# Optimization experiments

Hardware: AMD Instinct MI355X
Metric: run time of the kernel (lower is better)

The kernel has to match this reference:

```python
import jax, jax.numpy as jnp
import numpy as np
import math

B, C, H, W = 8, 512, 32, 32
NUM_GROUPS = 32
NUM_HEADS = C // 64  # num_head_channels=64 -> 8 heads
EPS = 1e-5


def setup_inputs() -> dict:
    key = jax.random.key(0)
    ks = jax.random.split(key, 7)
    x = jax.random.normal(ks[0], (B, C, H, W), dtype=jnp.float32)
    gn_w = jax.random.uniform(ks[1], (C,), dtype=jnp.float32, minval=0.5, maxval=1.5)
    gn_b = jax.random.normal(ks[2], (C,), dtype=jnp.float32) * 0.1
    qkv_w = jax.random.normal(ks[3], (3 * C, C), dtype=jnp.float32) * 0.02
    qkv_b = jax.random.normal(ks[4], (3 * C,), dtype=jnp.float32) * 0.02
    proj_w = jax.random.normal(ks[5], (C, C), dtype=jnp.float32) * 0.02
    proj_b = jax.random.normal(ks[6], (C,), dtype=jnp.float32) * 0.02
    return {"x": x, "gn_w": gn_w, "gn_b": gn_b, "qkv_w": qkv_w,
            "qkv_b": qkv_b, "proj_w": proj_w, "proj_b": proj_b}


def _group_norm(x, w, b):
    # x: [B, C, L]
    bb, cc, ll = x.shape
    g = x.reshape(bb, NUM_GROUPS, cc // NUM_GROUPS, ll)
    mean = g.mean(axis=(2, 3), keepdims=True)
    var = g.var(axis=(2, 3), keepdims=True)
    g = (g - mean) * jax.lax.rsqrt(var + EPS)
    return g.reshape(bb, cc, ll) * w[None, :, None] + b[None, :, None]


def reference(x, gn_w, gn_b, qkv_w, qkv_b, proj_w, proj_b):
    b, c, h, w = x.shape
    L = h * w
    xf = x.reshape(b, c, L)
    # 1x1 conv1d QKV on normalized input: weight [3C, C]
    qkv = jnp.einsum('oc,bcl->bol', qkv_w, _group_norm(xf, gn_w, gn_b)) + qkv_b[None, :, None]
    ch = c // NUM_HEADS  # per-head channels
    qkv = qkv.reshape(b * NUM_HEADS, 3 * ch, L)
    q, k, v = qkv[:, :ch], qkv[:, ch:2 * ch], qkv[:, 2 * ch:]
    scale = 1.0 / math.sqrt(math.sqrt(ch))
    # [b*H, T, S] scores, softmax over source dim (computed in fp32 per source)
    weight = jnp.einsum('bct,bcs->bts', q * scale, k * scale)
    weight = jax.nn.softmax(weight.astype(jnp.float32), axis=-1).astype(weight.dtype)
    a = jnp.einsum('bts,bcs->bct', weight, v).reshape(b, c, L)
    hproj = jnp.einsum('oc,bcl->bol', proj_w, a) + proj_b[None, :, None]
    return (xf + hproj).reshape(b, c, h, w)
```

## Files before the change

kernel.cpp:

```cpp
#include <hip/hip_runtime.h>
#include <math.h>

#define BB 8
#define CC 512
#define LL 1024
#define GG 32
#define CPG 16
#define NH 8
#define CH 64

typedef unsigned short ushort_t;
typedef __attribute__((ext_vector_type(8))) short short8;
typedef __attribute__((ext_vector_type(4))) float f32x4;
typedef __attribute__((ext_vector_type(16))) float f32x16;

#define SCALE_Q 0.18033688f

__device__ inline ushort_t f2bf(float f) {
  union { float f; unsigned u; } v;
  v.f = f;
  unsigned r = v.u + 0x7FFFu + ((v.u >> 16) & 1u);
  return (ushort_t)(r >> 16);
}

__device__ inline unsigned pack_bf2(float lo, float hi) {
  return __builtin_amdgcn_perm(__float_as_uint(hi), __float_as_uint(lo),
                               0x07060302u);
}

__device__ inline int swz(int r, int k) {
  return r * 64 + ((((k >> 3) ^ (r & 7)) << 3) | (k & 7));
}

__device__ inline int vswz(int c, int s) {
  return c * 128 + (s & 64) + ((((s >> 3) & 7) ^ (c & 7)) << 3) + (s & 7);
}

__device__ __forceinline__ void g2l16(const void* g, void* l) {
  __builtin_amdgcn_global_load_lds((const unsigned int*)g, (unsigned int*)l,
                                   16, 0, 0);
}

__global__ __launch_bounds__(512) void gnx_kernel(
    const float* __restrict__ x, const float* __restrict__ gn_w,
    const float* __restrict__ gn_b, const float* __restrict__ qkv_w,
    const float* __restrict__ proj_w, ushort_t* __restrict__ xnT,
    ushort_t* __restrict__ wq, ushort_t* __restrict__ wp) {
  if (blockIdx.x < BB * GG) {
    const int b = blockIdx.x / GG;
    const int g = blockIdx.x % GG;
    const int tid = threadIdx.x;
    const int ch = tid >> 5;
    const int lseg = tid & 31;
    __shared__ ushort_t Ts[1024 * 32];
    __shared__ float red[16];
    __shared__ float st[2];
    const float* xc = x + ((size_t)b * CC + (size_t)g * CPG + ch) * LL;
    float4 v[8];
    float sum = 0.f, sq = 0.f;
#pragma unroll
    for (int i = 0; i < 8; ++i) {
      v[i] = *(const float4*)(xc + lseg * 32 + i * 4);
      sum += (v[i].x + v[i].y) + (v[i].z + v[i].w);
      sq += (v[i].x * v[i].x + v[i].y * v[i].y) +
            (v[i].z * v[i].z + v[i].w * v[i].w);
    }
#pragma unroll
    for (int off = 32; off > 0; off >>= 1) {
      sum += __shfl_down(sum, off);
      sq += __shfl_down(sq, off);
    }
    const int wave = tid >> 6;
    if ((tid & 63) == 0) {
      red[wave] = sum;
      red[8 + wave] = sq;
    }
    __syncthreads();
    if (tid == 0) {
      float s = 0.f, q = 0.f;
#pragma unroll
      for (int i = 0; i < 8; ++i) {
        s += red[i];
        q += red[8 + i];
      }
      float mean = s * (1.f / (CPG * LL));
      float var = q * (1.f / (CPG * LL)) - mean * mean;
      st[0] = mean;
      st[1] = rsqrtf(var + 1e-5f);
    }
    __syncthreads();
    const int c = g * CPG + ch;
    const float sc = st[1] * gn_w[c];
    const float sh = gn_b[c] - st[0] * sc;
    const int chG = ch >> 3, ch7 = ch & 7;
#pragma unroll
    for (int i = 0; i < 8; ++i) {
      float vv[4] = {v[i].x, v[i].y, v[i].z, v[i].w};
#pragma unroll
      for (int j = 0; j < 4; ++j) {
        int l = lseg * 32 + i * 4 + j;
        int key = ((l >> 5) + (l >> 2)) & 3;
        int slot = (chG + key) & 3;
        Ts[l * 32 + slot * 8 + ch7] = f2bf(vv[j] * sc + sh);
      }
    }
    __syncthreads();
    const int cb64 = (g >> 2) * 64;
    const int grpb = (g & 3) * 2;
#pragma unroll
    for (int it = 0; it < 4; ++it) {
      int idx = tid + it * 512;
      int l = idx >> 1, gsel = idx & 1;
      int key = ((l >> 5) + (l >> 2)) & 3;
      int slot = (gsel + key) & 3;
      uint4 val = *(const uint4*)&Ts[l * 32 + slot * 8];
      int grp = (grpb + gsel) ^ (l & 7);
      *(uint4*)(xnT + ((size_t)b * LL + l) * CC + cb64 + grp * 8) = val;
    }
  } else {
    int cb = blockIdx.x - BB * GG;
    int idx = (cb * 512 + threadIdx.x) * 4;
    const int N1 = 3 * CC * CC;
    float4 v;
    ushort_t* mat;
    int row, k;
    if (idx < N1) {
      v = *(const float4*)(qkv_w + idx);
      row = idx >> 9;
      k = idx & 511;
      mat = wq + (size_t)row * CC;
    } else {
      int j = idx - N1;
      v = *(const float4*)(proj_w + j);
      row = j >> 9;
      k = j & 511;
      mat = wp + (size_t)row * CC;
    }
    int dcol = (k & ~63) | ((((k >> 3) & 7) ^ (row & 7)) << 3) | (k & 7);
    unsigned lo = f2bf(v.x) | ((unsigned)f2bf(v.y) << 16);
    unsigned hi = f2bf(v.z) | ((unsigned)f2bf(v.w) << 16);
    *(uint2*)(mat + dcol) = make_uint2(lo, hi);
  }
}

__global__ __launch_bounds__(384, 3) void qkv_mfma_kernel(
    const ushort_t* __restrict__ wq, const ushort_t* __restrict__ xnT,
    const float* __restrict__ qkv_b, ushort_t* __restrict__ qT,
    ushort_t* __restrict__ kT, ushort_t* __restrict__ vbuf) {
  const int b = blockIdx.z;
  const int m0 = blockIdx.y * 192;
  const int n0 = blockIdx.x * 128;
  const int tid = threadIdx.x;
  const int w = tid >> 6, lane = tid & 63;
  const int col = lane & 15, quad = lane >> 4;
  const int wm = (w >> 1) * 64, wn = (w & 1) * 64;
  __shared__ ushort_t Smem[2 * 20480];
  f32x4 acc[4][4];
  f32x4 z = {0.f, 0.f, 0.f, 0.f};
#pragma unroll
  for (int i = 0; i < 4; ++i)
#pragma unroll
    for (int j = 0; j < 4; ++j) acc[i][j] = z;

  const ushort_t* arow = wq + (size_t)m0 * CC;
  const ushort_t* brow = xnT + ((size_t)b * LL + n0) * CC;

  auto stage = [&](int bb, int k0) {
    ushort_t* As = Smem + bb * 20480;
    ushort_t* Bs = As + 12288;
#pragma unroll
    for (int j = 0; j < 4; ++j) {
      int e = (j * 6 + w) * 512 + lane * 8;
      g2l16(arow + (size_t)(e >> 6) * CC + k0 + (e & 63),
            As + (j * 6 + w) * 512);
    }
    if (w < 4) {
#pragma unroll
      for (int j = 0; j < 4; ++j) {
        int e = (j * 4 + w) * 512 + lane * 8;
        g2l16(brow + (size_t)(e >> 6) * CC + k0 + (e & 63),
              Bs + (j * 4 + w) * 512);
      }
    }
  };

  stage(0, 0);
  __syncthreads();
  int cur = 0;
  for (int step = 0; step < 8; ++step) {
    if (step < 7) stage(cur ^ 1, (step + 1) * 64);
    const ushort_t* As = Smem + cur * 20480;
    const ushort_t* Bs = As + 12288;
#pragma unroll
    for (int kk = 0; kk < 2; ++kk) {
      short8 af[4], bf[4];
#pragma unroll
      for (int mi = 0; mi < 4; ++mi)
        af[mi] = *(const short8*)&As[swz(wm + mi * 16 + col, kk * 32 + quad * 8)];
#pragma unroll
      for (int ni = 0; ni < 4; ++ni)
        bf[ni] = *(const short8*)&Bs[swz(wn + ni * 16 + col, kk * 32 + quad * 8)];
#pragma unroll
      for (int mi = 0; mi < 4; ++mi)
#pragma unroll
        for (int ni = 0; ni < 4; ++ni)
          acc[mi][ni] = __builtin_amdgcn_mfma_f32_16x16x32_bf16(
              af[mi], bf[ni], acc[mi][ni], 0, 0, 0);
    }
    __syncthreads();
    cur ^= 1;
  }
  const int ci_w = w >> 1;
  ushort_t* Tile = Smem + ci_w * 8192;
  if (ci_w < 2) {
    const float sc = (ci_w == 0) ? SCALE_Q : 1.f;
#pragma unroll
    for (int mi = 0; mi < 4; ++mi) {
      int mg = m0 + wm + mi * 16 + quad * 4;
      float b0 = qkv_b[mg + 0], b1 = qkv_b[mg + 1];
      float b2 = qkv_b[mg + 2], b3 = qkv_b[mg + 3];
      int ch = mi * 16 + quad * 4;
#pragma unroll
      for (int ni = 0; ni < 4; ++ni) {
        int lloc = wn + ni * 16 + col;
        float v0 = (acc[mi][ni][0] + b0) * sc;
        float v1 = (acc[mi][ni][1] + b1) * sc;
        float v2 = (acc[mi][ni][2] + b2) * sc;
        float v3 = (acc[mi][ni][3] + b3) * sc;
        int chs = ch ^ ((lloc & 7) << 3);
        *(uint2*)&Tile[lloc * 64 + chs] =
            make_uint2(pack_bf2(v0, v1), pack_bf2(v2, v3));
      }
    }
  } else {
#pragma unroll
    for (int mi = 0; mi < 4; ++mi)
#pragma unroll
      for (int r = 0; r < 4; ++r) {
        int ch = mi * 16 + quad * 4 + r;
        float bias = qkv_b[m0 + wm + ch];
#pragma unroll
        for (int ni = 0; ni < 4; ++ni) {
          int lloc = wn + ni * 16 + col;
          Tile[ch * 128 + lloc] =
              (ushort_t)(__float_as_uint(acc[mi][ni][r] + bias) >> 16);
        }
      }
  }
  __syncthreads();
  const int head = blockIdx.y;
  const int bh = b * NH + head;
#pragma unroll
  for (int ci = 0; ci < 3; ++ci) {
    ushort_t* T2 = Smem + ci * 8192;
    if (ci < 2) {
      ushort_t* dst = (ci == 0) ? qT : kT;
#pragma unroll
      for (int it = 0; it < 3; ++it) {
        int idx = tid + it * 384;
        if (idx < 1024) {
          int l = idx >> 3, seg = idx & 7;
          uint4 v = *(const uint4*)&T2[l * 64 + seg * 8];
          *(uint4*)(dst + ((size_t)bh * LL + n0 + l) * CH + seg * 8) = v;
        }
      }
    } else {
#pragma unroll
      for (int it = 0; it < 3; ++it) {
        int idx = tid + it * 384;
        if (idx < 1024) {
          int ch = idx >> 4, lseg = idx & 15;
          uint4 v = *(const uint4*)&T2[ch * 128 + lseg * 8];
          int g = lseg & 7, blk = lseg >> 3;
          *(uint4*)(vbuf + ((size_t)bh * CH + ch) * LL + n0 + blk * 64 +
                    ((g ^ (ch & 7)) << 3)) = v;
        }
      }
    }
  }
}

__global__ __launch_bounds__(256) void attn_mfma_kernel(
    const ushort_t* __restrict__ qT, const ushort_t* __restrict__ kT,
    const ushort_t* __restrict__ vbuf, ushort_t* __restrict__ abuf) {
  const int Bx = blockIdx.x;
  const int bh = (Bx & 7) * 8 + ((Bx >> 3) >> 3);
  const int t0g = ((Bx >> 3) & 7) * 128;
  const int b = bh >> 3, h = bh & 7;
  const int tid = threadIdx.x;
  const int w = tid >> 6, lane = tid & 63;
  const int ln31 = lane & 31, hi = lane >> 5;
  __shared__ ushort_t Ksm[2][128 * 64];
  __shared__ ushort_t Vsm[2][64 * 128];

  const ushort_t* kbase = kT + (size_t)bh * LL * CH;
  const ushort_t* vbase = vbuf + (size_t)bh * CH * LL;

#pragma unroll
  for (int i = 0; i < 4; ++i) {
    int e = i * 2048 + w * 512 + lane * 8;
    g2l16(kbase + e, &Ksm[0][i * 2048 + w * 512]);
    g2l16(vbase + (size_t)(e >> 7) * LL + (e & 127),
          &Vsm[0][i * 2048 + w * 512]);
  }
  const ushort_t* qtile = qT + ((size_t)bh * LL + t0g) * CH;
  short8 bq[4];
#pragma unroll
  for (int j = 0; j < 4; ++j)
    bq[j] = *(const short8*)&qtile[swz(w * 32 + ln31, j * 16 + hi * 8)];

  union { unsigned u[4]; short8 s; } onesu;
#pragma unroll
  for (int i = 0; i < 4; ++i) onesu.u[i] = 0x3F803F80u;
  const short8 bones = onesu.s;

  float m_s = 0.f;
  f32x16 oacc[2], osum;
  f32x16 zz = {0.f, 0.f, 0.f, 0.f, 0.f, 0.f, 0.f, 0.f,
               0.f, 0.f, 0.f, 0.f, 0.f, 0.f, 0.f, 0.f};
  oacc[0] = zz;
  oacc[1] = zz;
  osum = zz;
  __syncthreads();

  int cur = 0;
  for (int it2 = 0; it2 < 8; ++it2) {
    if (it2 < 7) {
#pragma unroll
      for (int i = 0; i < 4; ++i) {
        int e = i * 2048 + w * 512 + lane * 8;
        g2l16(kbase + (size_t)(it2 + 1) * 8192 + e,
              &Ksm[cur ^ 1][i * 2048 + w * 512]);
        g2l16(vbase + (size_t)(e >> 7) * LL + (it2 + 1) * 128 + (e & 127),
              &Vsm[cur ^ 1][i * 2048 + w * 512]);
      }
    }
    const ushort_t* Kc = Ksm[cur];
    const ushort_t* Vc = Vsm[cur];
#pragma unroll
    for (int h2 = 0; h2 < 2; ++h2) {
      f32x16 sacc[2];
      sacc[0] = zz;
      sacc[1] = zz;
      __builtin_amdgcn_s_setprio(1);
#pragma unroll
      for (int sq = 0; sq < 2; ++sq)
#pragma unroll
        for (int j = 0; j < 4; ++j) {
          short8 ak = *(const short8*)&Kc[swz(h2 * 64 + sq * 32 + ln31,
                                              j * 16 + hi * 8)];
          sacc[sq] = __builtin_amdgcn_mfma_f32_32x32x16_bf16(ak, bq[j],
                                                             sacc[sq], 0, 0, 0);
        }
      __builtin_amdgcn_s_setprio(0);
      if (it2 == 0 && h2 == 0) {
        float mx = sacc[0][0];
#pragma unroll
        for (int sq = 0; sq < 2; ++sq)
#pragma unroll
          for (int r = 0; r < 16; ++r) mx = fmaxf(mx, sacc[sq][r]);
#pragma unroll
        for (int off = 32; off > 0; off >>= 1)
          mx = fmaxf(mx, __shfl_xor(mx, off));
        m_s = mx;
      }
      short8 pf[4];
#pragma unroll
      for (int sq = 0; sq < 2; ++sq) {
        float p[16];
#pragma unroll
        for (int r = 0; r < 16; ++r)
          p[r] = __builtin_amdgcn_exp2f(sacc[sq][r] - m_s);
        unsigned d0[4], d1[4];
#pragma unroll
        for (int q = 0; q < 4; ++q) {
          d0[q] = pack_bf2(p[q * 4 + 0], p[q * 4 + 1]);
          d1[q] = pack_bf2(p[q * 4 + 2], p[q * 4 + 3]);
        }
#pragma unroll
        for (int m = 0; m < 2; ++m) {
          unsigned x0 = d0[m * 2], y0 = d0[m * 2 + 1];
          unsigned x1 = d1[m * 2], y1 = d1[m * 2 + 1];
          asm volatile("v_permlane32_swap_b32 %0, %1" : "+v"(x0), "+v"(y0));
          asm volatile("v_permlane32_swap_b32 %0, %1" : "+v"(x1), "+v"(y1));
          union { uint4 u; short8 s; } fu;
          fu.u = make_uint4(x0, x1, y0, y1);
          pf[sq * 2 + m] = fu.s;
        }
      }
      __builtin_amdgcn_s_setprio(1);
#pragma unroll
      for (int cq = 0; cq < 2; ++cq)
#pragma unroll
        for (int ks = 0; ks < 4; ++ks) {
          short8 bv = *(const short8*)&Vc[vswz(cq * 32 + ln31,
                                               h2 * 64 + ks * 16 + hi * 8)];
          oacc[cq] = __builtin_amdgcn_mfma_f32_32x32x16_bf16(pf[ks], bv,
                                                             oacc[cq], 0, 0, 0);
        }
#pragma unroll
      for (int ks = 0; ks < 4; ++ks)
        osum = __builtin_amdgcn_mfma_f32_32x32x16_bf16(pf[ks], bones, osum,
                                                       0, 0, 0);
      __builtin_amdgcn_s_setprio(0);
    }
    __syncthreads();
    cur ^= 1;
  }
#pragma unroll
  for (int r = 0; r < 16; ++r) {
    int tl = (r & 3) + 8 * (r >> 2) + 4 * hi;
    float li = 1.f / osum[r];
    int lg = t0g + w * 32 + tl;
#pragma unroll
    for (int cq = 0; cq < 2; ++cq) {
      int cl = cq * 32 + ln31;
      int dcol = ((((cl >> 3) ^ (lg & 7)) << 3) | (cl & 7));
      abuf[((size_t)b * LL + lg) * CC + h * CH + dcol] =
          f2bf(oacc[cq][r] * li);
    }
  }
}

__global__ __launch_bounds__(256) void proj_mfma_kernel(
    const ushort_t* __restrict__ wp, const ushort_t* __restrict__ abuf,
    const float* __restrict__ proj_b, const float* __restrict__ x,
    float* __restrict__ out) {
  const int b = blockIdx.z;
  const int m0 = blockIdx.y * 64;
  const int n0 = blockIdx.x * 128;
  const int tid = threadIdx.x;
  const int w = tid >> 6, lane = tid & 63;
  const int col = lane & 15, quad = lane >> 4;
  const int wm = (w >> 1) * 32, wn = (w & 1) * 64;
  __shared__ ushort_t Smem[2 * 12288];
  f32x4 acc[2][4];
  f32x4 z = {0.f, 0.f, 0.f, 0.f};
#pragma unroll
  for (int i = 0; i < 2; ++i)
#pragma unroll
    for (int j = 0; j < 4; ++j) acc[i][j] = z;

  const ushort_t* arow = wp + (size_t)m0 * CC;
  const ushort_t* brow = abuf + ((size_t)b * LL + n0) * CC;

  auto stage = [&](int bb, int k0) {
    ushort_t* As = Smem + bb * 12288;
    ushort_t* Bs = As + 4096;
#pragma unroll
    for (int j = 0; j < 2; ++j) {
      int e = (j * 4 + w) * 512 + lane * 8;
      g2l16(arow + (size_t)(e >> 6) * CC + k0 + (e & 63),
            As + (j * 4 + w) * 512);
    }
#pragma unroll
    for (int j = 0; j < 4; ++j) {
      int e = (j * 4 + w) * 512 + lane * 8;
      g2l16(brow + (size_t)(e >> 6) * CC + k0 + (e & 63),
            Bs + (j * 4 + w) * 512);
    }
  };

  stage(0, 0);
  __syncthreads();
  int cur = 0;
  for (int step = 0; step < 8; ++step) {
    if (step < 7) stage(cur ^ 1, (step + 1) * 64);
    const ushort_t* As = Smem + cur * 12288;
    const ushort_t* Bs = As + 4096;
#pragma unroll
    for (int kk = 0; kk < 2; ++kk) {
      short8 af[2], bf[4];
#pragma unroll
      for (int mi = 0; mi < 2; ++mi)
        af[mi] = *(const short8*)&As[swz(wm + mi * 16 + col, kk * 32 + quad * 8)];
#pragma unroll
      for (int ni = 0; ni < 4; ++ni)
        bf[ni] = *(const short8*)&Bs[swz(wn + ni * 16 + col, kk * 32 + quad * 8)];
#pragma unroll
      for (int mi = 0; mi < 2; ++mi)
#pragma unroll
        for (int ni = 0; ni < 4; ++ni)
          acc[mi][ni] = __builtin_amdgcn_mfma_f32_16x16x32_bf16(
              af[mi], bf[ni], acc[mi][ni], 0, 0, 0);
    }
    __syncthreads();
    cur ^= 1;
  }
#pragma unroll
  for (int mi = 0; mi < 2; ++mi)
#pragma unroll
    for (int r = 0; r < 4; ++r) {
      int o = m0 + wm + mi * 16 + quad * 4 + r;
      float bias = proj_b[o];
#pragma unroll
      for (int ni = 0; ni < 4; ++ni) {
        int l = n0 + wn + ni * 16 + col;
        size_t off = ((size_t)b * CC + o) * LL + l;
        out[off] = x[off] + bias + acc[mi][ni][r];
      }
    }
}

extern "C" void kernel_launch(void* const* d_in, const int* in_sizes, int n_in,
                              void* d_out, int out_size, void* d_ws,
                              size_t ws_size, hipStream_t stream) {
  const float* x = (const float*)d_in[0];
  const float* gn_w = (const float*)d_in[1];
  const float* gn_b = (const float*)d_in[2];
  const float* qkv_w = (const float*)d_in[3];
  const float* qkv_b = (const float*)d_in[4];
  const float* proj_w = (const float*)d_in[5];
  const float* proj_b = (const float*)d_in[6];
  float* out = (float*)d_out;

  char* ws = (char*)d_ws;
  ushort_t* wq = (ushort_t*)ws;
  ushort_t* wp = wq + (size_t)3 * CC * CC;
  ushort_t* xnT = wp + (size_t)CC * CC;
  ushort_t* qT = xnT + (size_t)BB * LL * CC;
  ushort_t* kT = qT + (size_t)BB * NH * LL * CH;
  ushort_t* vb = kT + (size_t)BB * NH * LL * CH;
  ushort_t* abuf = vb + (size_t)BB * NH * LL * CH;

  gnx_kernel<<<BB * GG + 512, 512, 0, stream>>>(x, gn_w, gn_b, qkv_w, proj_w,
                                                xnT, wq, wp);
  qkv_mfma_kernel<<<dim3(LL / 128, 1536 / 192, BB), 384, 0, stream>>>(
      wq, xnT, qkv_b, qT, kT, vb);
  attn_mfma_kernel<<<dim3(512), 256, 0, stream>>>(qT, kT, vb, abuf);
  proj_mfma_kernel<<<dim3(LL / 128, CC / 64, BB), 256, 0, stream>>>(
      wp, abuf, proj_b, x, out);
}
```

Baseline: 138.5 us.

## Use 4-stage K=32 LDS pipeline with 32-wide swizzle in QKV and proj GEMMs

Both GEMM kernels change from a double-buffered K=64 loop with full __syncthreads to a four-buffer ring of K=32 slices. Three slices are kept in flight, paced by explicit vmcnt waits and a single s_barrier per step. The global swizzle of xnT, the weights and abuf moves to a 32-column XOR pattern to match the new LDS tile width. The aim is to hide global-to-LDS latency better and cut barrier cost. In exchange there are twice as many loop iterations and hand-tuned vmcnt counts that must exactly match the number of outstanding loads.

```diff
diff --git a/kernel.cpp b/kernel.cpp
--- a/kernel.cpp
+++ b/kernel.cpp
@@ -16,6 +16,8 @@
 
 #define SCALE_Q 0.18033688f
 
+#define VMW(N) asm volatile("s_waitcnt vmcnt(" #N ")" ::: "memory")
+
 __device__ inline ushort_t f2bf(float f) {
   union { float f; unsigned u; } v;
   v.f = f;
@@ -30,6 +32,10 @@
 
 __device__ inline int swz(int r, int k) {
   return r * 64 + ((((k >> 3) ^ (r & 7)) << 3) | (k & 7));
+}
+
+__device__ inline int swz32(int r, int k) {
+  return r * 32 + (((((k >> 3) & 3) ^ ((r >> 1) & 3)) << 3) | (k & 7));
 }
 
 __device__ inline int vswz(int c, int s) {
@@ -105,8 +111,7 @@
       }
     }
     __syncthreads();
-    const int cb64 = (g >> 2) * 64;
-    const int grpb = (g & 3) * 2;
+    const int Gbase = g * 2;
 #pragma unroll
     for (int it = 0; it < 4; ++it) {
       int idx = tid + it * 512;
@@ -114,8 +119,9 @@
       int key = ((l >> 5) + (l >> 2)) & 3;
       int slot = (gsel + key) & 3;
       uint4 val = *(const uint4*)&Ts[l * 32 + slot * 8];
-      int grp = (grpb + gsel) ^ (l & 7);
-      *(uint4*)(xnT + ((size_t)b * LL + l) * CC + cb64 + grp * 8) = val;
+      int G = Gbase + gsel;
+      int pos = (G >> 2) * 32 + ((((G & 3) ^ ((l >> 1) & 3))) << 3);
+      *(uint4*)(xnT + ((size_t)b * LL + l) * CC + pos) = val;
     }
   } else {
     int cb = blockIdx.x - BB * GG;
@@ -136,7 +142,7 @@
       k = j & 511;
       mat = wp + (size_t)row * CC;
     }
-    int dcol = (k & ~63) | ((((k >> 3) & 7) ^ (row & 7)) << 3) | (k & 7);
+    int dcol = (k & ~31) | ((((k >> 3) & 3) ^ ((row >> 1) & 3)) << 3) | (k & 7);
     unsigned lo = f2bf(v.x) | ((unsigned)f2bf(v.y) << 16);
     unsigned hi = f2bf(v.z) | ((unsigned)f2bf(v.w) << 16);
     *(uint2*)(mat + dcol) = make_uint2(lo, hi);
@@ -154,7 +160,7 @@
   const int w = tid >> 6, lane = tid & 63;
   const int col = lane & 15, quad = lane >> 4;
   const int wm = (w >> 1) * 64, wn = (w & 1) * 64;
-  __shared__ ushort_t Smem[2 * 20480];
+  __shared__ ushort_t Smem[4 * 10240];
   f32x4 acc[4][4];
   f32x4 z = {0.f, 0.f, 0.f, 0.f};
 #pragma unroll
@@ -164,52 +170,59 @@
 
   const ushort_t* arow = wq + (size_t)m0 * CC;
   const ushort_t* brow = xnT + ((size_t)b * LL + n0) * CC;
+  const int srow = lane >> 2, scol = (lane & 3) * 8;
 
   auto stage = [&](int bb, int k0) {
-    ushort_t* As = Smem + bb * 20480;
-    ushort_t* Bs = As + 12288;
-#pragma unroll
-    for (int j = 0; j < 4; ++j) {
-      int e = (j * 6 + w) * 512 + lane * 8;
-      g2l16(arow + (size_t)(e >> 6) * CC + k0 + (e & 63),
-            As + (j * 6 + w) * 512);
+    ushort_t* As = Smem + bb * 10240;
+    ushort_t* Bs = As + 6144;
+#pragma unroll
+    for (int j = 0; j < 2; ++j) {
+      int s = w * 2 + j;
+      g2l16(arow + (size_t)(s * 16 + srow) * CC + k0 + scol, As + s * 512);
     }
     if (w < 4) {
 #pragma unroll
-      for (int j = 0; j < 4; ++j) {
-        int e = (j * 4 + w) * 512 + lane * 8;
-        g2l16(brow + (size_t)(e >> 6) * CC + k0 + (e & 63),
-              Bs + (j * 4 + w) * 512);
+      for (int j = 0; j < 2; ++j) {
+        int s = w * 2 + j;
+        g2l16(brow + (size_t)(s * 16 + srow) * CC + k0 + scol, Bs + s * 512);
       }
     }
   };
 
   stage(0, 0);
+  stage(1, 32);
+  stage(2, 64);
+  int cur = 0;
+  for (int step = 0; step < 16; ++step) {
+    if (step < 14) {
+      if (w < 4) VMW(8); else VMW(4);
+    } else if (step == 14) {
+      if (w < 4) VMW(4); else VMW(2);
+    } else {
+      VMW(0);
+    }
+    __builtin_amdgcn_sched_barrier(0);
+    __builtin_amdgcn_s_barrier();
+    __builtin_amdgcn_sched_barrier(0);
+    if (step < 13) stage((cur + 3) & 3, (step + 3) * 32);
+    const ushort_t* As = Smem + cur * 10240;
+    const ushort_t* Bs = As + 6144;
+    short8 af[4], bf[4];
+#pragma unroll
+    for (int mi = 0; mi < 4; ++mi)
+      af[mi] = *(const short8*)&As[swz32(wm + mi * 16 + col, quad * 8)];
+#pragma unroll
+    for (int ni = 0; ni < 4; ++ni)
+      bf[ni] = *(const short8*)&Bs[swz32(wn + ni * 16 + col, quad * 8)];
+#pragma unroll
+    for (int mi = 0; mi < 4; ++mi)
+#pragma unroll
+      for (int ni = 0; ni < 4; ++ni)
+        acc[mi][ni] = __builtin_amdgcn_mfma_f32_16x16x32_bf16(
+            af[mi], bf[ni], acc[mi][ni], 0, 0, 0);
+    cur = (cur + 1) & 3;
+  }
   __syncthreads();
-  int cur = 0;
-  for (int step = 0; step < 8; ++step) {
-    if (step < 7) stage(cur ^ 1, (step + 1) * 64);
-    const ushort_t* As = Smem + cur * 20480;
-    const ushort_t* Bs = As + 12288;
-#pragma unroll
-    for (int kk = 0; kk < 2; ++kk) {
-      short8 af[4], bf[4];
-#pragma unroll
-      for (int mi = 0; mi < 4; ++mi)
-        af[mi] = *(const short8*)&As[swz(wm + mi * 16 + col, kk * 32 + quad * 8)];
-#pragma unroll
-      for (int ni = 0; ni < 4; ++ni)
-        bf[ni] = *(const short8*)&Bs[swz(wn + ni * 16 + col, kk * 32 + quad * 8)];
-#pragma unroll
-      for (int mi = 0; mi < 4; ++mi)
-#pragma unroll
-        for (int ni = 0; ni < 4; ++ni)
-          acc[mi][ni] = __builtin_amdgcn_mfma_f32_16x16x32_bf16(
-              af[mi], bf[ni], acc[mi][ni], 0, 0, 0);
-    }
-    __syncthreads();
-    cur ^= 1;
-  }
   const int ci_w = w >> 1;
   ushort_t* Tile = Smem + ci_w * 8192;
   if (ci_w < 2) {
@@ -415,8 +428,9 @@
 #pragma unroll
     for (int cq = 0; cq < 2; ++cq) {
       int cl = cq * 32 + ln31;
-      int dcol = ((((cl >> 3) ^ (lg & 7)) << 3) | (cl & 7));
-      abuf[((size_t)b * LL + lg) * CC + h * CH + dcol] =
+      int pos = (cl & 32) | ((((cl >> 3) & 3) ^ ((lg >> 1) & 3)) << 3) |
+                (cl & 7);
+      abuf[((size_t)b * LL + lg) * CC + h * CH + pos] =
           f2bf(oacc[cq][r] * li);
     }
   }
@@ -433,7 +447,7 @@
   const int w = tid >> 6, lane = tid & 63;
   const int col = lane & 15, quad = lane >> 4;
   const int wm = (w >> 1) * 32, wn = (w & 1) * 64;
-  __shared__ ushort_t Smem[2 * 12288];
+  __shared__ ushort_t Smem[4 * 6144];
   f32x4 acc[2][4];
   f32x4 z = {0.f, 0.f, 0.f, 0.f};
 #pragma unroll
@@ -443,49 +457,47 @@
 
   const ushort_t* arow = wp + (size_t)m0 * CC;
   const ushort_t* brow = abuf + ((size_t)b * LL + n0) * CC;
+  const int srow = lane >> 2, scol = (lane & 3) * 8;
 
   auto stage = [&](int bb, int k0) {
-    ushort_t* As = Smem + bb * 12288;
-    ushort_t* Bs = As + 4096;
+    ushort_t* As = Smem + bb * 6144;
+    ushort_t* Bs = As + 2048;
+    g2l16(arow + (size_t)(w * 16 + srow) * CC + k0 + scol, As + w * 512);
 #pragma unroll
     for (int j = 0; j < 2; ++j) {
-      int e = (j * 4 + w) * 512 + lane * 8;
-      g2l16(arow + (size_t)(e >> 6) * CC + k0 + (e & 63),
-            As + (j * 4 + w) * 512);
-    }
-#pragma unroll
-    for (int j = 0; j < 4; ++j) {
-      int e = (j * 4 + w) * 512 + lane * 8;
-      g2l16(brow + (size_t)(e >> 6) * CC + k0 + (e & 63),
-            Bs + (j * 4 + w) * 512);
+      int s = w * 2 + j;
+      g2l16(brow + (size_t)(s * 16 + srow) * CC + k0 + scol, Bs + s * 512);
     }
   };
 
   stage(0, 0);
-  __syncthreads();
+  stage(1, 32);
+  stage(2, 64);
   int cur = 0;
-  for (int step = 0; step < 8; ++step) {
-    if (step < 7) stage(cur ^ 1, (step + 1) * 64);
-    const ushort_t* As = Smem + cur * 12288;
-    const ushort_t* Bs = As + 4096;
-#pragma unroll
-    for (int kk = 0; kk < 2; ++kk) {
-      short8 af[2], bf[4];
-#pragma unroll
-      for (int mi = 0; mi < 2; ++mi)
-        af[mi] = *(const short8*)&As[swz(wm + mi * 16 + col, kk * 32 + quad * 8)];
+  for (int step = 0; step < 16; ++step) {
+    if (step < 14) VMW(6);
+    else if (step == 14) VMW(3);
+    else VMW(0);
+    __builtin_amdgcn_sched_barrier(0);
+    __builtin_amdgcn_s_barrier();
+    __builtin_amdgcn_sched_barrier(0);
+    if (step < 13) stage((cur + 3) & 3, (step + 3) * 32);
+    const ushort_t* As = Smem + cur * 6144;
+    const ushort_t* Bs = As + 2048;
+    short8 af[2], bf[4];
+#pragma unroll
+    for (int mi = 0; mi < 2; ++mi)
+      af[mi] = *(const short8*)&As[swz32(wm + mi * 16 + col, quad * 8)];
+#pragma unroll
+    for (int ni = 0; ni < 4; ++ni)
+      bf[ni] = *(const short8*)&Bs[swz32(wn + ni * 16 + col, quad * 8)];
+#pragma unroll
+    for (int mi = 0; mi < 2; ++mi)
 #pragma unroll
       for (int ni = 0; ni < 4; ++ni)
-        bf[ni] = *(const short8*)&Bs[swz(wn + ni * 16 + col, kk * 32 + quad * 8)];
-#pragma unroll
-      for (int mi = 0; mi < 2; ++mi)
-#pragma unroll
-        for (int ni = 0; ni < 4; ++ni)
-          acc[mi][ni] = __builtin_amdgcn_mfma_f32_16x16x32_bf16(
-              af[mi], bf[ni], acc[mi][ni], 0, 0, 0);
-    }
-    __syncthreads();
-    cur ^= 1;
+        acc[mi][ni] = __builtin_amdgcn_mfma_f32_16x16x32_bf16(
+            af[mi], bf[ni], acc[mi][ni], 0, 0, 0);
+    cur = (cur + 1) & 3;
   }
 #pragma unroll
   for (int mi = 0; mi < 2; ++mi)
```

New measurement: 142.5 us. +2.9%, slower.
